# Kernel optimization log

Measured on AMD Instinct MI355X. Metric: run time of the kernel, lower is better.

## Reference

```python
import jax, jax.numpy as jnp
import numpy as np

T, B, I, H, O = 512, 64, 256, 512, 256

def setup_inputs() -> dict:
    key = jax.random.key(0)
    ks = jax.random.split(key, 7)
    s_ih = 1.0 / np.sqrt(H)
    return {
        "x": jax.random.normal(ks[0], (T, B, I), dtype=jnp.float32),
        "W_ih": jax.random.uniform(ks[1], (H, I), jnp.float32, -s_ih, s_ih),
        "W_hh": jax.random.uniform(ks[2], (H, H), jnp.float32, -s_ih, s_ih),
        "b_ih": jax.random.uniform(ks[3], (H,), jnp.float32, -s_ih, s_ih),
        "b_hh": jax.random.uniform(ks[4], (H,), jnp.float32, -s_ih, s_ih),
        "W_out": jax.random.uniform(ks[5], (O, H), jnp.float32, -s_ih, s_ih),
        "b_out": jax.random.uniform(ks[6], (O,), jnp.float32, -s_ih, s_ih),
    }

def reference(x, W_ih, W_hh, b_ih, b_hh, W_out, b_out):
    # Precompute input projection for all timesteps: [T, B, H]
    xp = jnp.einsum('tbi,hi->tbh', x, W_ih) + b_ih + b_hh

    def step(h, xp_t):
        h_new = jnp.tanh(xp_t + h @ W_hh.T)
        return h_new, h_new

    h0 = jnp.zeros((x.shape[1], W_hh.shape[0]), dtype=x.dtype)
    h_last, rnn_out = jax.lax.scan(step, h0, xp)  # rnn_out: [T, B, H]
    y = jnp.einsum('tbh,oh->tbo', rnn_out, W_out) + b_out
    return y, h_last[None]  # h: [1, B, H] matching torch nn.RNN
```

## Files before the change

kernel.cpp:

```cpp
#include <hip/hip_runtime.h>

#define T_DIM 512
#define B_DIM 64
#define I_DIM 256
#define H_DIM 512
#define O_DIM 256

typedef __attribute__((ext_vector_type(8))) short short8;
typedef __attribute__((ext_vector_type(4))) float f32x4;
typedef __attribute__((ext_vector_type(4))) int   i32x4;

__device__ __forceinline__ unsigned short f2bf(float f){
  unsigned int u = __builtin_bit_cast(unsigned int, f);
  u += 0x7fffu + ((u >> 16) & 1u);
  return (unsigned short)(u >> 16);
}
__device__ __forceinline__ float bf2f(unsigned short b){
  unsigned int u = ((unsigned int)b) << 16;
  return __builtin_bit_cast(float, u);
}

#if defined(__has_builtin)
#if __has_builtin(__builtin_amdgcn_update_dpp)
#define HAVE_DPP 1
#endif
#endif

__global__ void pack_bf16(const float* __restrict__ x,
                          const float* __restrict__ wih,
                          const float* __restrict__ wout,
                          unsigned short* __restrict__ xb,
                          unsigned short* __restrict__ wihb,
                          unsigned short* __restrict__ woutb){
  const int NX = (T_DIM*B_DIM*I_DIM)/4;
  const int NW = (H_DIM*I_DIM)/4;
  int i = blockIdx.x * 256 + threadIdx.x;
  const float4* src; unsigned short* dst; int j;
  if (i < NX)          { src = (const float4*)x;    dst = xb;    j = i; }
  else if (i < NX+NW)  { src = (const float4*)wih;  dst = wihb;  j = i - NX; }
  else                 { src = (const float4*)wout; dst = woutb; j = i - NX - NW; }
  float4 f = src[j];
  ushort4 v;
  v.x = f2bf(f.x); v.y = f2bf(f.y); v.z = f2bf(f.z); v.w = f2bf(f.w);
  ((ushort4*)dst)[j] = v;
}

__global__ void quant_whh(const float* __restrict__ W, int* __restrict__ Wq){
  int p = blockIdx.x * blockDim.x + threadIdx.x;
  const float s  = 0.04419417382415922f;
  const float qs = 127.0f / s;
  int out = 0;
  #pragma unroll
  for (int i = 0; i < 4; ++i){
    float w = W[(size_t)p*4 + i];
    int q = __float2int_rn(w * qs);
    q = q < -127 ? -127 : (q > 127 ? 127 : q);
    out |= (q & 0xff) << (8*i);
  }
  Wq[p] = out;
}

__global__
__attribute__((amdgpu_flat_work_group_size(512, 512), amdgpu_waves_per_eu(2, 2)))
void rnn_recur(
    const int* __restrict__ Wq,
    const unsigned short* __restrict__ xp,
    unsigned short* __restrict__ rnn,
    float* __restrict__ hlast)
{
  __shared__ union {
    char H[2][512];
    char occupancy_cap[84 * 1024];
  } sm;
  const int b    = blockIdx.x;
  const int tid  = threadIdx.x;
  const int lane = tid & 63;
  const int wv   = tid >> 6;
  const int lr   = lane & 15;
  const int hi   = lane >> 4;

  i32x4 wf[4][8];
  const char* Wb = (const char*)Wq;
  #pragma unroll
  for (int rt = 0; rt < 4; ++rt){
    const char* rowp = Wb + (size_t)(64*wv + 16*rt + lr)*512 + hi*16;
    #pragma unroll
    for (int kt = 0; kt < 8; ++kt)
      wf[rt][kt] = *(const i32x4*)(rowp + (size_t)kt*64);
  }

  if (tid < 256) ((int*)sm.H)[tid] = 0;

  const int src = (((lane >> 2) & 3) << 4) | ((lane >> 4) << 2) | (lane & 3);

  const float kscale = 0.04419417382415922f / (127.0f * 127.0f);
  const int BH = B_DIM * H_DIM;

  float xp_next = bf2f(xp[(size_t)b*H_DIM + tid]);
  float h = 0.0f;
  __syncthreads();

  for (int t = 0; t < T_DIM; ++t){
    float xp_cur = xp_next;
    {
      int tn = (t + 1 < T_DIM) ? (t + 1) : t;
      xp_next = bf2f(xp[(size_t)tn*BH + (size_t)b*H_DIM + tid]);
    }

    const char* Hc = sm.H[t & 1];
    i32x4 a0 = {0,0,0,0}, a1 = {0,0,0,0}, a2 = {0,0,0,0}, a3 = {0,0,0,0};
    #pragma unroll
    for (int kt = 0; kt < 8; ++kt){
      i32x4 bf = *(const i32x4*)(Hc + kt*64 + hi*16);
      a0 = __builtin_amdgcn_mfma_i32_16x16x64_i8(wf[0][kt], bf, a0, 0, 0, 0);
      a1 = __builtin_amdgcn_mfma_i32_16x16x64_i8(wf[1][kt], bf, a1, 0, 0, 0);
      a2 = __builtin_amdgcn_mfma_i32_16x16x64_i8(wf[2][kt], bf, a2, 0, 0, 0);
      a3 = __builtin_amdgcn_mfma_i32_16x16x64_i8(wf[3][kt], bf, a3, 0, 0, 0);
    }

    int f0, f1, f2, f3;
    {
      int e0 = (lane & 4) ? a1[0] : a0[0];
      int e1 = (lane & 4) ? a3[0] : a2[0];
      f0 = (lane & 8) ? e1 : e0;
      e0 = (lane & 4) ? a1[1] : a0[1];
      e1 = (lane & 4) ? a3[1] : a2[1];
      f1 = (lane & 8) ? e1 : e0;
      e0 = (lane & 4) ? a1[2] : a0[2];
      e1 = (lane & 4) ? a3[2] : a2[2];
      f2 = (lane & 8) ? e1 : e0;
      e0 = (lane & 4) ? a1[3] : a0[3];
      e1 = (lane & 4) ? a3[3] : a2[3];
      f3 = (lane & 8) ? e1 : e0;
    }
    int g0 = (lane & 1) ? f1 : f0;
    int g1 = (lane & 1) ? f3 : f2;
    int am0 = (lane & 2) ? g1 : g0;
    int am  = __shfl(am0, src);

    float pre = xp_cur + (float)am * kscale;
    float aa = fabsf(pre);
    float e  = __expf(-2.0f * aa);
    float r  = (1.0f - e) * __builtin_amdgcn_rcpf(1.0f + e);
    h = copysignf(r, pre);

    rnn[(size_t)t*BH + (size_t)b*H_DIM + tid] = f2bf(h);

    int q = __float2int_rn(h * 127.0f) & 0xff;
#ifdef HAVE_DPP
    int p1 = __builtin_amdgcn_update_dpp(0, q, 0xB1, 0xf, 0xf, true);
    int y  = q | (p1 << 8);
    int p2 = __builtin_amdgcn_update_dpp(0, y, 0x4E, 0xf, 0xf, true);
    int z  = y | (p2 << 16);
    if ((tid & 3) == 0) ((int*)sm.H[(t + 1) & 1])[tid >> 2] = z;
#else
    sm.H[(t + 1) & 1][tid] = (char)q;
#endif
    __syncthreads();
  }
  hlast[(size_t)b*H_DIM + tid] = h;
}

template<typename TA, typename TB, typename TO>
__global__ __launch_bounds__(256) void gemm_bt(
    const TA* __restrict__ A, const TB* __restrict__ B, TO* __restrict__ C,
    const float* __restrict__ bias1, const float* __restrict__ bias2,
    int M, int N, int K)
{
  __shared__ unsigned short As[64][40];
  __shared__ unsigned short Bs[64][40];
  const int tid  = threadIdx.x;
  const int m0   = blockIdx.y * 64;
  const int n0   = blockIdx.x * 64;
  const int srow = tid >> 2, skc = tid & 3;
  const int lane = tid & 63, wid = tid >> 6;
  const int wm   = wid >> 1, wn = wid & 1;
  const int lr   = lane & 15, lq = lane >> 4;

  f32x4 acc[2][2];
  #pragma unroll
  for (int i = 0; i < 2; ++i)
    #pragma unroll
    for (int j = 0; j < 2; ++j) acc[i][j] = (f32x4){0.f, 0.f, 0.f, 0.f};

  for (int k0 = 0; k0 < K; k0 += 32){
    {
      const TA* src = A + (size_t)(m0 + srow)*K + k0 + skc*8;
      uint4 v;
      if constexpr (__is_same(TA, float)){
        float4 f0 = *(const float4*)src;
        float4 f1 = *(const float4*)(src + 4);
        v.x = (unsigned)f2bf(f0.x) | ((unsigned)f2bf(f0.y) << 16);
        v.y = (unsigned)f2bf(f0.z) | ((unsigned)f2bf(f0.w) << 16);
        v.z = (unsigned)f2bf(f1.x) | ((unsigned)f2bf(f1.y) << 16);
        v.w = (unsigned)f2bf(f1.z) | ((unsigned)f2bf(f1.w) << 16);
      } else {
        v = *(const uint4*)src;
      }
      *(uint4*)&As[srow][skc*8] = v;
    }
    {
      const TB* src = B + (size_t)(n0 + srow)*K + k0 + skc*8;
      uint4 v;
      if constexpr (__is_same(TB, float)){
        float4 f0 = *(const float4*)src;
        float4 f1 = *(const float4*)(src + 4);
        v.x = (unsigned)f2bf(f0.x) | ((unsigned)f2bf(f0.y) << 16);
        v.y = (unsigned)f2bf(f0.z) | ((unsigned)f2bf(f0.w) << 16);
        v.z = (unsigned)f2bf(f1.x) | ((unsigned)f2bf(f1.y) << 16);
        v.w = (unsigned)f2bf(f1.z) | ((unsigned)f2bf(f1.w) << 16);
      } else {
        v = *(const uint4*)src;
      }
      *(uint4*)&Bs[srow][skc*8] = v;
    }
    __syncthreads();
    uint4 av0 = *(const uint4*)&As[wm*32      + lr][lq*8];
    uint4 av1 = *(const uint4*)&As[wm*32 + 16 + lr][lq*8];
    uint4 bv0 = *(const uint4*)&Bs[wn*32      + lr][lq*8];
    uint4 bv1 = *(const uint4*)&Bs[wn*32 + 16 + lr][lq*8];
    short8 a0 = __builtin_bit_cast(short8, av0);
    short8 a1 = __builtin_bit_cast(short8, av1);
    short8 b0 = __builtin_bit_cast(short8, bv0);
    short8 b1 = __builtin_bit_cast(short8, bv1);
    acc[0][0] = __builtin_amdgcn_mfma_f32_16x16x32_bf16(a0, b0, acc[0][0], 0, 0, 0);
    acc[0][1] = __builtin_amdgcn_mfma_f32_16x16x32_bf16(a0, b1, acc[0][1], 0, 0, 0);
    acc[1][0] = __builtin_amdgcn_mfma_f32_16x16x32_bf16(a1, b0, acc[1][0], 0, 0, 0);
    acc[1][1] = __builtin_amdgcn_mfma_f32_16x16x32_bf16(a1, b1, acc[1][1], 0, 0, 0);
    __syncthreads();
  }

  #pragma unroll
  for (int i = 0; i < 2; ++i)
    #pragma unroll
    for (int j = 0; j < 2; ++j)
      #pragma unroll
      for (int r = 0; r < 4; ++r){
        int grow = m0 + wm*32 + i*16 + lq*4 + r;
        int gcol = n0 + wn*32 + j*16 + lr;
        float v = acc[i][j][r] + bias1[gcol];
        if (bias2) v += bias2[gcol];
        if constexpr (__is_same(TO, float)) C[(size_t)grow*N + gcol] = v;
        else                                C[(size_t)grow*N + gcol] = f2bf(v);
      }
}

extern "C" void kernel_launch(void* const* d_in, const int* in_sizes, int n_in,
                              void* d_out, int out_size, void* d_ws, size_t ws_size,
                              hipStream_t stream){
  (void)in_sizes; (void)n_in; (void)out_size; (void)ws_size;
  const float* x    = (const float*)d_in[0];
  const float* Wih  = (const float*)d_in[1];
  const float* Whh  = (const float*)d_in[2];
  const float* bih  = (const float*)d_in[3];
  const float* bhh  = (const float*)d_in[4];
  const float* Wout = (const float*)d_in[5];
  const float* bout = (const float*)d_in[6];
  float* y     = (float*)d_out;
  float* hlast = y + (size_t)T_DIM * B_DIM * O_DIM;

  char* ws = (char*)d_ws;
  const size_t MB = 1024*1024;
  unsigned short* xp   = (unsigned short*)ws;
  unsigned short* rnn  = (unsigned short*)(ws + 32*MB);
  unsigned short* xb   = (unsigned short*)(ws + 32*MB);
  unsigned short* wihb = (unsigned short*)(ws + 48*MB);
  int*            Wq   = (int*)           (ws + 64*MB);
  unsigned short* wob  = (unsigned short*)(ws + 64*MB + 256*1024);

  pack_bf16<<<8448, 256, 0, stream>>>(x, Wih, Wout, xb, wihb, wob);
  quant_whh<<<256, 256, 0, stream>>>(Whh, Wq);
  gemm_bt<unsigned short, unsigned short, unsigned short><<<dim3(8, 512), 256, 0, stream>>>(
      xb, wihb, xp, bih, bhh, T_DIM*B_DIM, H_DIM, I_DIM);
  rnn_recur<<<64, 512, 0, stream>>>(Wq, xp, rnn, hlast);
  gemm_bt<unsigned short, unsigned short, float><<<dim3(4, 512), 256, 0, stream>>>(
      rnn, wob, y, bout, nullptr, T_DIM*B_DIM, O_DIM, H_DIM);
}
```

Before: 524.2 us.

## Split recurrent matvec between MFMA and sdot4 VALU dot products per wave

Each wave now computes half of its 64 output rows with int8 MFMA and the other half with VALU sdot4 dot products over weights held in registers. The two lane halves each reduce a 256-element half and combine with a cross-lane xor shuffle. The aim is to shorten the serial per-step MFMA chain by running VALU work alongside the matrix unit. The cost is 64 extra weight registers per lane, more LDS reads of the hidden state, and more VALU instructions on the critical path.

```diff
diff --git a/kernel.cpp b/kernel.cpp
--- a/kernel.cpp
+++ b/kernel.cpp
@@ -21,10 +21,25 @@
 }
 
 #if defined(__has_builtin)
+#if __has_builtin(__builtin_amdgcn_sdot4)
+#define HAVE_SDOT4 1
+#endif
 #if __has_builtin(__builtin_amdgcn_update_dpp)
 #define HAVE_DPP 1
 #endif
 #endif
+
+__device__ __forceinline__ int sdot4(int a, int b, int c){
+#ifdef HAVE_SDOT4
+  return __builtin_amdgcn_sdot4(a, b, c, false);
+#else
+  #pragma unroll
+  for (int i = 0; i < 4; ++i){
+    c += (int)(signed char)(a >> (8*i) & 0xff) * (int)(signed char)(b >> (8*i) & 0xff);
+  }
+  return c;
+#endif
+}
 
 __global__ void pack_bf16(const float* __restrict__ x,
                           const float* __restrict__ wih,
@@ -78,20 +93,32 @@
   const int wv   = tid >> 6;
   const int lr   = lane & 15;
   const int hi   = lane >> 4;
-
-  i32x4 wf[4][8];
+  const int ch   = lane >> 5;
+
   const char* Wb = (const char*)Wq;
-  #pragma unroll
-  for (int rt = 0; rt < 4; ++rt){
+
+  i32x4 wf[2][8];
+  #pragma unroll
+  for (int rt = 0; rt < 2; ++rt){
     const char* rowp = Wb + (size_t)(64*wv + 16*rt + lr)*512 + hi*16;
     #pragma unroll
     for (int kt = 0; kt < 8; ++kt)
       wf[rt][kt] = *(const i32x4*)(rowp + (size_t)kt*64);
   }
+  int wd[64];
+  {
+    const uint4* wp = (const uint4*)(Wb + (size_t)(64*wv + 32 + (lane & 31))*512 + ch*256);
+    #pragma unroll
+    for (int k = 0; k < 16; ++k){
+      uint4 v = wp[k];
+      wd[4*k+0] = (int)v.x; wd[4*k+1] = (int)v.y;
+      wd[4*k+2] = (int)v.z; wd[4*k+3] = (int)v.w;
+    }
+  }
 
   if (tid < 256) ((int*)sm.H)[tid] = 0;
 
-  const int src = (((lane >> 2) & 3) << 4) | ((lane >> 4) << 2) | (lane & 3);
+  const int srcm = (lane & 3) | (((lane >> 4) & 1) << 2) | (((lane >> 2) & 3) << 4);
 
   const float kscale = 0.04419417382415922f / (127.0f * 127.0f);
   const int BH = B_DIM * H_DIM;
@@ -108,35 +135,39 @@
     }
 
     const char* Hc = sm.H[t & 1];
-    i32x4 a0 = {0,0,0,0}, a1 = {0,0,0,0}, a2 = {0,0,0,0}, a3 = {0,0,0,0};
+
+    i32x4 a0 = {0,0,0,0}, a1 = {0,0,0,0};
     #pragma unroll
     for (int kt = 0; kt < 8; ++kt){
       i32x4 bf = *(const i32x4*)(Hc + kt*64 + hi*16);
       a0 = __builtin_amdgcn_mfma_i32_16x16x64_i8(wf[0][kt], bf, a0, 0, 0, 0);
       a1 = __builtin_amdgcn_mfma_i32_16x16x64_i8(wf[1][kt], bf, a1, 0, 0, 0);
-      a2 = __builtin_amdgcn_mfma_i32_16x16x64_i8(wf[2][kt], bf, a2, 0, 0, 0);
-      a3 = __builtin_amdgcn_mfma_i32_16x16x64_i8(wf[3][kt], bf, a3, 0, 0, 0);
-    }
-
-    int f0, f1, f2, f3;
+    }
+
+    int dacc = 0;
     {
-      int e0 = (lane & 4) ? a1[0] : a0[0];
-      int e1 = (lane & 4) ? a3[0] : a2[0];
-      f0 = (lane & 8) ? e1 : e0;
-      e0 = (lane & 4) ? a1[1] : a0[1];
-      e1 = (lane & 4) ? a3[1] : a2[1];
-      f1 = (lane & 8) ? e1 : e0;
-      e0 = (lane & 4) ? a1[2] : a0[2];
-      e1 = (lane & 4) ? a3[2] : a2[2];
-      f2 = (lane & 8) ? e1 : e0;
-      e0 = (lane & 4) ? a1[3] : a0[3];
-      e1 = (lane & 4) ? a3[3] : a2[3];
-      f3 = (lane & 8) ? e1 : e0;
-    }
-    int g0 = (lane & 1) ? f1 : f0;
-    int g1 = (lane & 1) ? f3 : f2;
-    int am0 = (lane & 2) ? g1 : g0;
-    int am  = __shfl(am0, src);
+      const uint4* hp = (const uint4*)(Hc + ch*256);
+      #pragma unroll
+      for (int k = 0; k < 16; ++k){
+        uint4 hv = hp[k];
+        dacc = sdot4(wd[4*k+0], (int)hv.x, dacc);
+        dacc = sdot4(wd[4*k+1], (int)hv.y, dacc);
+        dacc = sdot4(wd[4*k+2], (int)hv.z, dacc);
+        dacc = sdot4(wd[4*k+3], (int)hv.w, dacc);
+      }
+    }
+    dacc += __shfl_xor(dacc, 32);
+
+    int e0 = (lane & 4) ? a1[0] : a0[0];
+    int e1 = (lane & 4) ? a1[1] : a0[1];
+    int e2 = (lane & 4) ? a1[2] : a0[2];
+    int e3 = (lane & 4) ? a1[3] : a0[3];
+    int g0 = (lane & 1) ? e1 : e0;
+    int g1 = (lane & 1) ? e3 : e2;
+    int v  = (lane & 2) ? g1 : g0;
+    int mm = __shfl(v, srcm);
+
+    int am = (lane & 32) ? dacc : mm;
 
     float pre = xp_cur + (float)am * kscale;
     float aa = fabsf(pre);
```

Result: slower. 623.2 us (+18.9%).

## Split recurrent matvec between MFMA waves and sdot4 VALU waves

Applied to the files above, without the earlier changes.

Waves 0-3 keep the int8 MFMA path for their hidden rows, while waves 4-7 compute their rows with per-lane sdot4 dot products over the whole 512-wide int8 hidden vector held in registers. The aim is to spread each step's small matvec across both the matrix and vector units so less time is spent waiting on MFMA issue and latency per timestep. The VALU path needs 32 LDS broadcast loads and 128 sdot4 per lane each step, which could lengthen the critical path. It also adds divergent per-wave code paths inside the serial loop.

```diff
diff --git a/kernel.cpp b/kernel.cpp
--- a/kernel.cpp
+++ b/kernel.cpp
@@ -21,10 +21,25 @@
 }
 
 #if defined(__has_builtin)
+#if __has_builtin(__builtin_amdgcn_sdot4)
+#define HAVE_SDOT4 1
+#endif
 #if __has_builtin(__builtin_amdgcn_update_dpp)
 #define HAVE_DPP 1
 #endif
 #endif
+
+__device__ __forceinline__ int sdot4(int a, int b, int c){
+#ifdef HAVE_SDOT4
+  return __builtin_amdgcn_sdot4(a, b, c, false);
+#else
+  #pragma unroll
+  for (int i = 0; i < 4; ++i){
+    c += (int)(signed char)(a >> (8*i) & 0xff) * (int)(signed char)(b >> (8*i) & 0xff);
+  }
+  return c;
+#endif
+}
 
 __global__ void pack_bf16(const float* __restrict__ x,
                           const float* __restrict__ wih,
@@ -76,22 +91,31 @@
   const int tid  = threadIdx.x;
   const int lane = tid & 63;
   const int wv   = tid >> 6;
+  const bool mat = (wv < 4);
   const int lr   = lane & 15;
   const int hi   = lane >> 4;
 
-  i32x4 wf[4][8];
   const char* Wb = (const char*)Wq;
-  #pragma unroll
-  for (int rt = 0; rt < 4; ++rt){
-    const char* rowp = Wb + (size_t)(64*wv + 16*rt + lr)*512 + hi*16;
+
+  i32x4 wreg[32];
+  if (mat){
     #pragma unroll
-    for (int kt = 0; kt < 8; ++kt)
-      wf[rt][kt] = *(const i32x4*)(rowp + (size_t)kt*64);
+    for (int rt = 0; rt < 4; ++rt){
+      const char* rowp = Wb + (size_t)(64*wv + 16*rt + lr)*512 + hi*16;
+      #pragma unroll
+      for (int kt = 0; kt < 8; ++kt)
+        wreg[rt*8 + kt] = *(const i32x4*)(rowp + (size_t)kt*64);
+    }
+  } else {
+    const char* rowp = Wb + (size_t)(64*wv + lane)*512;
+    #pragma unroll
+    for (int k = 0; k < 32; ++k)
+      wreg[k] = *(const i32x4*)(rowp + k*16);
   }
 
   if (tid < 256) ((int*)sm.H)[tid] = 0;
 
-  const int src = (((lane >> 2) & 3) << 4) | ((lane >> 4) << 2) | (lane & 3);
+  const int srcm = (((lane >> 2) & 3) << 4) | ((lane >> 4) << 2) | (lane & 3);
 
   const float kscale = 0.04419417382415922f / (127.0f * 127.0f);
   const int BH = B_DIM * H_DIM;
@@ -108,35 +132,48 @@
     }
 
     const char* Hc = sm.H[t & 1];
-    i32x4 a0 = {0,0,0,0}, a1 = {0,0,0,0}, a2 = {0,0,0,0}, a3 = {0,0,0,0};
-    #pragma unroll
-    for (int kt = 0; kt < 8; ++kt){
-      i32x4 bf = *(const i32x4*)(Hc + kt*64 + hi*16);
-      a0 = __builtin_amdgcn_mfma_i32_16x16x64_i8(wf[0][kt], bf, a0, 0, 0, 0);
-      a1 = __builtin_amdgcn_mfma_i32_16x16x64_i8(wf[1][kt], bf, a1, 0, 0, 0);
-      a2 = __builtin_amdgcn_mfma_i32_16x16x64_i8(wf[2][kt], bf, a2, 0, 0, 0);
-      a3 = __builtin_amdgcn_mfma_i32_16x16x64_i8(wf[3][kt], bf, a3, 0, 0, 0);
-    }
-
-    int f0, f1, f2, f3;
-    {
-      int e0 = (lane & 4) ? a1[0] : a0[0];
-      int e1 = (lane & 4) ? a3[0] : a2[0];
-      f0 = (lane & 8) ? e1 : e0;
-      e0 = (lane & 4) ? a1[1] : a0[1];
-      e1 = (lane & 4) ? a3[1] : a2[1];
-      f1 = (lane & 8) ? e1 : e0;
-      e0 = (lane & 4) ? a1[2] : a0[2];
-      e1 = (lane & 4) ? a3[2] : a2[2];
-      f2 = (lane & 8) ? e1 : e0;
-      e0 = (lane & 4) ? a1[3] : a0[3];
-      e1 = (lane & 4) ? a3[3] : a2[3];
-      f3 = (lane & 8) ? e1 : e0;
-    }
-    int g0 = (lane & 1) ? f1 : f0;
-    int g1 = (lane & 1) ? f3 : f2;
-    int am0 = (lane & 2) ? g1 : g0;
-    int am  = __shfl(am0, src);
+    int am;
+    if (mat){
+      i32x4 a0 = {0,0,0,0}, a1 = {0,0,0,0}, a2 = {0,0,0,0}, a3 = {0,0,0,0};
+      #pragma unroll
+      for (int kt = 0; kt < 8; ++kt){
+        i32x4 bf = *(const i32x4*)(Hc + kt*64 + hi*16);
+        a0 = __builtin_amdgcn_mfma_i32_16x16x64_i8(wreg[ 0 + kt], bf, a0, 0, 0, 0);
+        a1 = __builtin_amdgcn_mfma_i32_16x16x64_i8(wreg[ 8 + kt], bf, a1, 0, 0, 0);
+        a2 = __builtin_amdgcn_mfma_i32_16x16x64_i8(wreg[16 + kt], bf, a2, 0, 0, 0);
+        a3 = __builtin_amdgcn_mfma_i32_16x16x64_i8(wreg[24 + kt], bf, a3, 0, 0, 0);
+      }
+      int f0, f1, f2, f3;
+      {
+        int e0 = (lane & 4) ? a1[0] : a0[0];
+        int e1 = (lane & 4) ? a3[0] : a2[0];
+        f0 = (lane & 8) ? e1 : e0;
+        e0 = (lane & 4) ? a1[1] : a0[1];
+        e1 = (lane & 4) ? a3[1] : a2[1];
+        f1 = (lane & 8) ? e1 : e0;
+        e0 = (lane & 4) ? a1[2] : a0[2];
+        e1 = (lane & 4) ? a3[2] : a2[2];
+        f2 = (lane & 8) ? e1 : e0;
+        e0 = (lane & 4) ? a1[3] : a0[3];
+        e1 = (lane & 4) ? a3[3] : a2[3];
+        f3 = (lane & 8) ? e1 : e0;
+      }
+      int g0 = (lane & 1) ? f1 : f0;
+      int g1 = (lane & 1) ? f3 : f2;
+      int v  = (lane & 2) ? g1 : g0;
+      am = __shfl(v, srcm);
+    } else {
+      int dacc = 0;
+      #pragma unroll
+      for (int k = 0; k < 32; ++k){
+        i32x4 hv = *(const i32x4*)(Hc + k*16);
+        dacc = sdot4(wreg[k][0], hv[0], dacc);
+        dacc = sdot4(wreg[k][1], hv[1], dacc);
+        dacc = sdot4(wreg[k][2], hv[2], dacc);
+        dacc = sdot4(wreg[k][3], hv[3], dacc);
+      }
+      am = dacc;
+    }
 
     float pre = xp_cur + (float)am * kscale;
     float aa = fabsf(pre);
```

Result: slower. 670.6 us (+27.9%).
